# Optimization experiments

Measured on AMD Instinct MI355X. Metric: run time of the kernel, lower is better.

The kernel has to match this reference:

```python
import jax, jax.numpy as jnp
import numpy as np

B, S, D, H, V, C = 64, 512, 512, 512, 32000, 1000
FF = 1024

def setup_inputs() -> dict:
    key = jax.random.key(0)
    ks = jax.random.split(key, 12)
    s = 0.02
    return {
        "tokens": jax.random.randint(ks[0], (B, S), 0, V),
        "emb": jax.random.normal(ks[1], (V, D), jnp.float32) * s,
        "Wx": jax.random.normal(ks[2], (D, H), jnp.float32) * s,
        "Wh": jax.random.normal(ks[3], (H, H), jnp.float32) * s,
        "b_rnn": jnp.zeros((H,), jnp.float32),
        "W1": jax.random.normal(ks[4], (H, FF), jnp.float32) * s,
        "b1": jnp.zeros((FF,), jnp.float32),
        "W2": jax.random.normal(ks[5], (FF, FF), jnp.float32) * s,
        "b2": jnp.zeros((FF,), jnp.float32),
        "Wo": jax.random.normal(ks[6], (FF, C), jnp.float32) * s,
        "bo": jnp.zeros((C,), jnp.float32),
    }

def reference(tokens, emb, Wx, Wh, b_rnn, W1, b1, W2, b2, Wo, bo):
    # Embedding with mask_zero=True: token 0 is a masked timestep
    x = emb[tokens]                                   # [B,S,D]
    mask = (tokens != 0)                              # [B,S]
    # Precompute input projection for all timesteps (hoisted out of the scan)
    xproj = jnp.einsum('bsd,dh->bsh', x, Wx) + b_rnn  # [B,S,H]

    def step(h, inp):
        xp, m = inp                                   # [B,H], [B]
        h_new = jax.nn.relu(xp + h @ Wh)
        # Keras masking: masked steps carry previous state forward
        h = jnp.where(m[:, None], h_new, h)
        return h, None

    h0 = jnp.zeros((B, H), xproj.dtype)
    h, _ = jax.lax.scan(step, h0, (xproj.transpose(1, 0, 2), mask.T))

    y = jax.nn.relu(h @ W1 + b1)
    y = jax.nn.relu(y @ W2 + b2)
    return jax.nn.softmax(y @ Wo + bo, axis=-1)       # [B,C]
```

## Files before the change

kernel.cpp:

```cpp
#include <hip/hip_runtime.h>
#include <stdint.h>

typedef _Float16 half2_t __attribute__((ext_vector_type(2)));
typedef short bf16x8 __attribute__((ext_vector_type(8)));
typedef float f32x4 __attribute__((ext_vector_type(4)));
typedef int i32x4 __attribute__((ext_vector_type(4)));
typedef int i32x8 __attribute__((ext_vector_type(8)));
typedef unsigned short u16;
typedef unsigned int u32;
typedef unsigned long long u64;

#define B_ 64
#define S_ 512
#define D_ 512
#define H_ 512
#define FF_ 1024
#define C_ 1000
#define V_ 32000

#define SW4 128.0f
#define SH4 256.0f

__device__ __forceinline__ u16 f2bf(float f){
  u32 u = __builtin_bit_cast(u32, f);
  u = (u + 0x7FFFu + ((u >> 16) & 1u)) >> 16;
  return (u16)u;
}
__device__ __forceinline__ u32 pkbf(float a, float b){
  return (u32)f2bf(a) | ((u32)f2bf(b) << 16);
}
__device__ __forceinline__ u32 packh2(float a, float b){
  u16 lo = __builtin_bit_cast(u16, (_Float16)a);
  u16 hi = __builtin_bit_cast(u16, (_Float16)b);
  return (u32)lo | ((u32)hi << 16);
}
__device__ __forceinline__ float fdot2u(u32 a, u32 b, float c){
  return __builtin_amdgcn_fdot2(__builtin_bit_cast(half2_t, a),
                                __builtin_bit_cast(half2_t, b), c, false);
}
__device__ __forceinline__ float h2f(u16 h){
  return (float)__builtin_bit_cast(_Float16, h);
}
__device__ __forceinline__ float fp4val(u32 c){
  int e = (c >> 1) & 3;
  float m = 1.0f + 0.5f * (float)(c & 1);
  return (e == 0) ? 0.5f * (float)(c & 1) : m * (float)(1 << (e - 1));
}

__global__ void k_prep(const float* __restrict__ Wx, u16* __restrict__ WxT,
                       const float* __restrict__ Wh, uint4* __restrict__ Wf4){
  __shared__ u16 t[64][65];
  int bid = blockIdx.x, tid = threadIdx.x;
  if (bid < 64){
    int bx = bid & 7, by = bid >> 3;
    int c = tid & 63, r0 = (tid >> 6) * 16;
    #pragma unroll
    for (int i = 0; i < 16; i++){
      int k = by * 64 + r0 + i, n = bx * 64 + c;
      t[r0 + i][c] = f2bf(Wx[k * 512 + n]);
    }
    __syncthreads();
    #pragma unroll
    for (int i = 0; i < 16; i++){
      int n = bx * 64 + r0 + i, k = by * 64 + c;
      WxT[n * 512 + k] = t[c][r0 + i];
    }
  } else {
    int g = (bid - 64) * 256 + tid;
    int fidx = g >> 6, l = g & 63;
    int wv = fidx >> 4, ct = (fidx >> 2) & 3, kt = fidx & 3;
    int q = l >> 4, n = wv * 64 + ct * 16 + (l & 15);
    int k0 = kt * 128 + q * 32;
    u32 d[4] = {0u, 0u, 0u, 0u};
    #pragma unroll
    for (int j = 0; j < 32; j++){
      float w = Wh[(size_t)(k0 + j) * 512 + n] * SW4;
      float aw = fabsf(w);
      u32 s = (w < 0.f) ? 8u : 0u;
      u32 c;
      if (aw < 2.f) c = (u32)(int)rintf(aw * 2.f);
      else if (aw < 4.f) c = 4u + (u32)(int)rintf(aw - 2.f);
      else { c = 6u + (u32)(int)rintf((aw - 4.f) * 0.5f); if (c > 7u) c = 7u; }
      d[j >> 3] |= (c | s) << (4 * (j & 7));
    }
    uint4 o; o.x = d[0]; o.y = d[1]; o.z = d[2]; o.w = d[3];
    Wf4[(size_t)fidx * 64 + l] = o;
  }
}

__global__ __launch_bounds__(512) void k_gemm(const float* __restrict__ emb,
                                              const u16* __restrict__ WxT,
                                              const float* __restrict__ bias,
                                              u16* __restrict__ xpV,
                                              const float* __restrict__ W1, u32* __restrict__ W1p,
                                              const float* __restrict__ W2, u32* __restrict__ W2p,
                                              const float* __restrict__ Wo, u32* __restrict__ Wop){
  __shared__ __align__(16) u16 As[64 * 40];
  int bid = blockIdx.x, tid = threadIdx.x;
  if (bid >= 500){
    if (bid < 1012){
      int i = (bid - 500) * 512 + tid;
      int p = i >> 10, n = i & 1023;
      W1p[p * FF_ + n] = packh2(W1[(2 * p) * FF_ + n], W1[(2 * p + 1) * FF_ + n]);
    } else if (bid < 2036){
      int i = (bid - 1012) * 512 + tid;
      int p = i >> 10, n = i & 1023;
      W2p[p * FF_ + n] = packh2(W2[(2 * p) * FF_ + n], W2[(2 * p + 1) * FF_ + n]);
    } else {
      int i = (bid - 2036) * 512 + tid;
      int p = i >> 10, n = i & 1023;
      if (n < C_)
        Wop[p * C_ + n] = packh2(Wo[(2 * p) * C_ + n], Wo[(2 * p + 1) * C_ + n]);
    }
    return;
  }
  int m0 = bid * 64;
  int w = tid >> 6, l = tid & 63, kg = l >> 4, r16 = l & 15;
  const u16* bptr[4];
  #pragma unroll
  for (int ni = 0; ni < 4; ni++)
    bptr[ni] = WxT + (size_t)(w * 64 + ni * 16 + r16) * 512 + kg * 8;
  f32x4 acc[4][4];
  #pragma unroll
  for (int mi = 0; mi < 4; mi++)
    #pragma unroll
    for (int ni = 0; ni < 4; ni++) acc[mi][ni] = (f32x4){0.f, 0.f, 0.f, 0.f};
  int srow = tid >> 3, sk = (tid & 7) * 4;
  const float* ebase = emb + (size_t)(m0 + srow) * 512 + sk;
  float4 f = *(const float4*)ebase;
  for (int kt = 0; kt < 16; kt++){
    u32 lo = pkbf(f.x, f.y), hi = pkbf(f.z, f.w);
    float4 fn;
    if (kt < 15) fn = *(const float4*)(ebase + (kt + 1) * 32);
    __syncthreads();
    uint2 st; st.x = lo; st.y = hi;
    *(uint2*)(As + srow * 40 + sk) = st;
    __syncthreads();
    bf16x8 bfr[4], af[4];
    #pragma unroll
    for (int ni = 0; ni < 4; ni++)
      bfr[ni] = *(const bf16x8*)(bptr[ni] + kt * 32);
    #pragma unroll
    for (int mi = 0; mi < 4; mi++)
      af[mi] = *(const bf16x8*)(As + (mi * 16 + r16) * 40 + kg * 8);
    #pragma unroll
    for (int mi = 0; mi < 4; mi++)
      #pragma unroll
      for (int ni = 0; ni < 4; ni++)
        acc[mi][ni] = __builtin_amdgcn_mfma_f32_16x16x32_bf16(af[mi], bfr[ni], acc[mi][ni], 0, 0, 0);
    f = fn;
  }
  #pragma unroll
  for (int ni = 0; ni < 4; ni++){
    int col = w * 64 + ni * 16 + r16;
    float bb = bias[col];
    #pragma unroll
    for (int mi = 0; mi < 4; mi++){
      int mb = m0 + mi * 16 + kg * 4;
      #pragma unroll
      for (int r = 0; r < 4; r++){
        float v = (acc[mi][ni][r] + bb) * SH4;
        xpV[(size_t)(mb + r) * 512 + col] = __builtin_bit_cast(u16, (_Float16)v);
      }
    }
  }
}

__global__ __launch_bounds__(512, 2) void k_rnn(
    const uint4* __restrict__ Wf4, const u16* __restrict__ xpV,
    const int* __restrict__ tokens, u32* __restrict__ hpack){
  __shared__ __align__(16) unsigned char gA[256];
  __shared__ __align__(16) unsigned char gB[256];
  __shared__ int toks[512];
  int b = blockIdx.x, tid = threadIdx.x;
  int wv = tid >> 6, l = tid & 63, q = l >> 4, n16 = l & 15;
  int col = wv * 64 + q * 16 + n16;

  i32x8 wgt[16];
  #pragma unroll
  for (int ct = 0; ct < 4; ct++)
    #pragma unroll
    for (int kt = 0; kt < 4; kt++){
      int fidx = (wv * 4 + ct) * 4 + kt;
      uint4 wl = Wf4[(size_t)fidx * 64 + l];
      i32x8 w8 = {(int)wl.x, (int)wl.y, (int)wl.z, (int)wl.w, 0, 0, 0, 0};
      wgt[ct * 4 + kt] = w8;
    }

  toks[tid] = tokens[b * 512 + tid];
  if (tid < 64) ((u32*)gA)[tid] = 0;
  __syncthreads();

  const u16* xpc = xpV + col;
  u16 xraw = xpc[(size_t)toks[0] * 512];
  u32 greg = 0;

#define RNN_STEP(T, SRC, DST)                                                 \
  {                                                                           \
    int tn = toks[(T + 1) & 511];                                             \
    u16 xnext = xpc[(size_t)tn * 512];                                        \
    bool wr = toks[T] != 0;                                                   \
    i32x4 av0 = *(const i32x4*)(SRC + 0 * 64 + q * 16);                       \
    i32x4 av1 = *(const i32x4*)(SRC + 1 * 64 + q * 16);                       \
    i32x4 av2 = *(const i32x4*)(SRC + 2 * 64 + q * 16);                       \
    i32x4 av3 = *(const i32x4*)(SRC + 3 * 64 + q * 16);                       \
    i32x8 a80 = {av0[0], av0[1], av0[2], av0[3], 0, 0, 0, 0};                 \
    i32x8 a81 = {av1[0], av1[1], av1[2], av1[3], 0, 0, 0, 0};                 \
    i32x8 a82 = {av2[0], av2[1], av2[2], av2[3], 0, 0, 0, 0};                 \
    i32x8 a83 = {av3[0], av3[1], av3[2], av3[3], 0, 0, 0, 0};                 \
    f32x4 acc0 = {0.f,0.f,0.f,0.f}, acc1 = {0.f,0.f,0.f,0.f};                 \
    f32x4 acc2 = {0.f,0.f,0.f,0.f}, acc3 = {0.f,0.f,0.f,0.f};                 \
    __builtin_amdgcn_s_setprio(1);                                            \
    acc0 = __builtin_amdgcn_mfma_scale_f32_16x16x128_f8f6f4(a80, wgt[0],  acc0, 4, 4, 0, 127, 0, 127); \
    acc1 = __builtin_amdgcn_mfma_scale_f32_16x16x128_f8f6f4(a80, wgt[4],  acc1, 4, 4, 0, 127, 0, 127); \
    acc2 = __builtin_amdgcn_mfma_scale_f32_16x16x128_f8f6f4(a80, wgt[8],  acc2, 4, 4, 0, 127, 0, 127); \
    acc3 = __builtin_amdgcn_mfma_scale_f32_16x16x128_f8f6f4(a80, wgt[12], acc3, 4, 4, 0, 127, 0, 127); \
    acc0 = __builtin_amdgcn_mfma_scale_f32_16x16x128_f8f6f4(a81, wgt[1],  acc0, 4, 4, 0, 127, 0, 127); \
    acc1 = __builtin_amdgcn_mfma_scale_f32_16x16x128_f8f6f4(a81, wgt[5],  acc1, 4, 4, 0, 127, 0, 127); \
    acc2 = __builtin_amdgcn_mfma_scale_f32_16x16x128_f8f6f4(a81, wgt[9],  acc2, 4, 4, 0, 127, 0, 127); \
    acc3 = __builtin_amdgcn_mfma_scale_f32_16x16x128_f8f6f4(a81, wgt[13], acc3, 4, 4, 0, 127, 0, 127); \
    acc0 = __builtin_amdgcn_mfma_scale_f32_16x16x128_f8f6f4(a82, wgt[2],  acc0, 4, 4, 0, 127, 0, 127); \
    acc1 = __builtin_amdgcn_mfma_scale_f32_16x16x128_f8f6f4(a82, wgt[6],  acc1, 4, 4, 0, 127, 0, 127); \
    acc2 = __builtin_amdgcn_mfma_scale_f32_16x16x128_f8f6f4(a82, wgt[10], acc2, 4, 4, 0, 127, 0, 127); \
    acc3 = __builtin_amdgcn_mfma_scale_f32_16x16x128_f8f6f4(a82, wgt[14], acc3, 4, 4, 0, 127, 0, 127); \
    acc0 = __builtin_amdgcn_mfma_scale_f32_16x16x128_f8f6f4(a83, wgt[3],  acc0, 4, 4, 0, 127, 0, 127); \
    acc1 = __builtin_amdgcn_mfma_scale_f32_16x16x128_f8f6f4(a83, wgt[7],  acc1, 4, 4, 0, 127, 0, 127); \
    acc2 = __builtin_amdgcn_mfma_scale_f32_16x16x128_f8f6f4(a83, wgt[11], acc2, 4, 4, 0, 127, 0, 127); \
    acc3 = __builtin_amdgcn_mfma_scale_f32_16x16x128_f8f6f4(a83, wgt[15], acc3, 4, 4, 0, 127, 0, 127); \
    __builtin_amdgcn_s_setprio(0);                                            \
    float av = (q == 0) ? acc0[0] : (q == 1) ? acc1[0] : (q == 2) ? acc2[0] : acc3[0]; \
    float gn = fmaxf(fmaf(av, 1.0f / SW4, h2f(xraw)), 0.f);                   \
    u32 code;                                                                 \
    if (gn < 2.f) code = (u32)(int)rintf(gn * 2.f);                           \
    else if (gn < 4.f) code = 4u + (u32)(int)rintf(gn - 2.f);                 \
    else { u32 c = 6u + (u32)(int)rintf((gn - 4.f) * 0.5f); code = c > 7u ? 7u : c; } \
    u32 pc = (u32)__shfl_xor((int)code, 1);                                   \
    u32 byte = (n16 & 1) ? (pc | (code << 4)) : (code | (pc << 4));           \
    if (wr) greg = byte;                                                      \
    if ((l & 1) == 0) DST[col >> 1] = (unsigned char)greg;                    \
    xraw = xnext;                                                             \
  }

  #pragma unroll 1
  for (int t = 0; t < 512; t += 2){
    RNN_STEP(t, gA, gB);
    __syncthreads();
    RNN_STEP(t + 1, gB, gA);
    __syncthreads();
  }
#undef RNN_STEP

  if (tid < 256){
    u32 byte = gA[tid];
    float f0 = fp4val(byte & 15u) * (1.0f / SH4);
    float f1 = fp4val(byte >> 4) * (1.0f / SH4);
    hpack[b * 256 + tid] = packh2(f0, f1);
  }
}

__global__ __launch_bounds__(256) void k_fc1(const u32* __restrict__ hpack,
    const u32* __restrict__ W1p, const float* __restrict__ b1, u32* __restrict__ y1p){
  __shared__ u32 h0[256], h1[256];
  int nx = blockIdx.x, bp = blockIdx.y, tid = threadIdx.x;
  int ba = bp * 2, bb = ba + 1;
  int n = nx * 256 + tid;
  h0[tid] = hpack[ba * 256 + tid];
  h1[tid] = hpack[bb * 256 + tid];
  __syncthreads();
  float a0 = 0.f, a1 = 0.f;
  #pragma unroll 8
  for (int p = 0; p < 256; p++){
    u32 w = W1p[p * FF_ + n];
    a0 = fdot2u(w, h0[p], a0);
    a1 = fdot2u(w, h1[p], a1);
  }
  float bbv = b1[n];
  float y0 = fmaxf(a0 + bbv, 0.f), y1 = fmaxf(a1 + bbv, 0.f);
  float o0 = __shfl_xor(y0, 1), o1 = __shfl_xor(y1, 1);
  if (!(tid & 1)){
    y1p[ba * 512 + (n >> 1)] = packh2(y0, o0);
    y1p[bb * 512 + (n >> 1)] = packh2(y1, o1);
  }
}

__global__ __launch_bounds__(256) void k_fc2(const u32* __restrict__ y1p,
    const u32* __restrict__ W2p, const float* __restrict__ b2, u32* __restrict__ y2p){
  __shared__ u32 h0[512], h1[512];
  int nx = blockIdx.x, bp = blockIdx.y, tid = threadIdx.x;
  int ba = bp * 2, bb = ba + 1;
  int n = nx * 256 + tid;
  h0[tid] = y1p[ba * 512 + tid];       h1[tid] = y1p[bb * 512 + tid];
  h0[tid + 256] = y1p[ba * 512 + 256 + tid];
  h1[tid + 256] = y1p[bb * 512 + 256 + tid];
  __syncthreads();
  float a0 = 0.f, a1 = 0.f;
  #pragma unroll 8
  for (int p = 0; p < 512; p++){
    u32 w = W2p[p * FF_ + n];
    a0 = fdot2u(w, h0[p], a0);
    a1 = fdot2u(w, h1[p], a1);
  }
  float bbv = b2[n];
  float y0 = fmaxf(a0 + bbv, 0.f), y1 = fmaxf(a1 + bbv, 0.f);
  float o0 = __shfl_xor(y0, 1), o1 = __shfl_xor(y1, 1);
  if (!(tid & 1)){
    y2p[ba * 512 + (n >> 1)] = packh2(y0, o0);
    y2p[bb * 512 + (n >> 1)] = packh2(y1, o1);
  }
}

__global__ __launch_bounds__(256) void k_outz(const u32* __restrict__ y2p,
    const u32* __restrict__ Wop, const float* __restrict__ bo, float* __restrict__ z){
  __shared__ u32 h0[512], h1[512];
  int nx = blockIdx.x, bp = blockIdx.y, tid = threadIdx.x;
  int ba = bp * 2, bb = ba + 1;
  h0[tid] = y2p[ba * 512 + tid];       h1[tid] = y2p[bb * 512 + tid];
  h0[tid + 256] = y2p[ba * 512 + 256 + tid];
  h1[tid + 256] = y2p[bb * 512 + 256 + tid];
  __syncthreads();
  int n = nx * 250 + tid;
  if (tid >= 250) return;
  float a0 = 0.f, a1 = 0.f;
  #pragma unroll 8
  for (int p = 0; p < 512; p++){
    u32 w = Wop[p * C_ + n];
    a0 = fdot2u(w, h0[p], a0);
    a1 = fdot2u(w, h1[p], a1);
  }
  float bbv = bo[n];
  z[ba * C_ + n] = a0 + bbv;
  z[bb * C_ + n] = a1 + bbv;
}

__global__ __launch_bounds__(256) void k_norm(const float* __restrict__ z,
                                              float* __restrict__ out){
  __shared__ float redm[4], reds[4];
  int b = blockIdx.x, tid = threadIdx.x;
  float z0 = z[b * C_ + tid];
  float z1 = z[b * C_ + 256 + tid];
  float z2 = z[b * C_ + 512 + tid];
  bool v3 = (768 + tid) < C_;
  float z3 = v3 ? z[b * C_ + 768 + tid] : -1e30f;
  float mx = fmaxf(fmaxf(z0, z1), fmaxf(z2, z3));
  #pragma unroll
  for (int o = 1; o < 64; o <<= 1) mx = fmaxf(mx, __shfl_xor(mx, o));
  if ((tid & 63) == 0) redm[tid >> 6] = mx;
  __syncthreads();
  mx = fmaxf(fmaxf(redm[0], redm[1]), fmaxf(redm[2], redm[3]));
  float e0 = __expf(z0 - mx), e1 = __expf(z1 - mx), e2 = __expf(z2 - mx);
  float e3 = v3 ? __expf(z3 - mx) : 0.f;
  float s = e0 + e1 + e2 + e3;
  #pragma unroll
  for (int o = 1; o < 64; o <<= 1) s += __shfl_xor(s, o);
  if ((tid & 63) == 0) reds[tid >> 6] = s;
  __syncthreads();
  s = reds[0] + reds[1] + reds[2] + reds[3];
  float inv = 1.0f / s;
  out[b * C_ + tid] = e0 * inv;
  out[b * C_ + 256 + tid] = e1 * inv;
  out[b * C_ + 512 + tid] = e2 * inv;
  if (v3) out[b * C_ + 768 + tid] = e3 * inv;
}

extern "C" void kernel_launch(void* const* d_in, const int* in_sizes, int n_in,
                              void* d_out, int out_size, void* d_ws, size_t ws_size,
                              hipStream_t stream) {
  const int*   tokens = (const int*)d_in[0];
  const float* emb    = (const float*)d_in[1];
  const float* Wx     = (const float*)d_in[2];
  const float* Wh     = (const float*)d_in[3];
  const float* brnn   = (const float*)d_in[4];
  const float* W1     = (const float*)d_in[5];
  const float* b1     = (const float*)d_in[6];
  const float* W2     = (const float*)d_in[7];
  const float* b2     = (const float*)d_in[8];
  const float* Wo     = (const float*)d_in[9];
  const float* bo     = (const float*)d_in[10];
  float* out = (float*)d_out;

  char* ws = (char*)d_ws;
  size_t off = 0;
  auto alloc = [&](size_t bytes) -> void* {
    void* p = ws + off;
    off += (bytes + 255) & ~(size_t)255;
    return p;
  };
  u16* WxT    = (u16*)alloc((size_t)512 * 512 * 2);
  u16* xpV    = (u16*)alloc((size_t)V_ * 512 * 2);
  uint4* Wf4  = (uint4*)alloc((size_t)128 * 64 * 16);
  u32* W1p    = (u32*)alloc((size_t)256 * 1024 * 4);
  u32* W2p    = (u32*)alloc((size_t)512 * 1024 * 4);
  u32* Wop    = (u32*)alloc((size_t)512 * 1000 * 4);
  u32* hpack  = (u32*)alloc((size_t)64 * 256 * 4);
  u32* y1p    = (u32*)alloc((size_t)64 * 512 * 4);
  u32* y2p    = (u32*)alloc((size_t)64 * 512 * 4);
  float* zbuf = (float*)alloc((size_t)64 * 1000 * 4);

  k_prep<<<dim3(96), dim3(256), 0, stream>>>(Wx, WxT, Wh, Wf4);
  k_gemm<<<dim3(3060), dim3(512), 0, stream>>>(emb, WxT, brnn, xpV,
                                               W1, W1p, W2, W2p, Wo, Wop);
  k_rnn<<<dim3(64), dim3(512), 0, stream>>>(Wf4, xpV, tokens, hpack);
  k_fc1<<<dim3(4, 32), dim3(256), 0, stream>>>(hpack, W1p, b1, y1p);
  k_fc2<<<dim3(4, 32), dim3(256), 0, stream>>>(y1p, W2p, b2, y2p);
  k_outz<<<dim3(4, 32), dim3(256), 0, stream>>>(y2p, Wop, bo, zbuf);
  k_norm<<<dim3(64), dim3(256), 0, stream>>>(zbuf, out);
}
```

Before: 377.3 us.

## Fuse FC1, FC2, output and softmax into one kernel with per-pair barriers

Replaces four tail launches (fc1, fc2, outz, norm) with a single 128-block kernel. Each group of 4 blocks sharing a batch pair synchronizes through a global atomic counter barrier between stages. The counters are zeroed in the gemm kernel. This removes three kernel launch gaps at the cost of spin-wait barriers, which depend on all 128 blocks being co-resident.

Result: slower. 421.9 us (+11.8%).

```diff
diff --git a/kernel.cpp b/kernel.cpp
--- a/kernel.cpp
+++ b/kernel.cpp
@@ -94,10 +94,12 @@
                                               u16* __restrict__ xpV,
                                               const float* __restrict__ W1, u32* __restrict__ W1p,
                                               const float* __restrict__ W2, u32* __restrict__ W2p,
-                                              const float* __restrict__ Wo, u32* __restrict__ Wop){
+                                              const float* __restrict__ Wo, u32* __restrict__ Wop,
+                                              u32* __restrict__ sync){
   __shared__ __align__(16) u16 As[64 * 40];
   int bid = blockIdx.x, tid = threadIdx.x;
   if (bid >= 500){
+    if (bid == 500 && tid < 128) sync[tid] = 0;
     if (bid < 1012){
       int i = (bid - 500) * 512 + tid;
       int p = i >> 10, n = i & 1023;
@@ -258,108 +260,125 @@
   }
 }
 
-__global__ __launch_bounds__(256) void k_fc1(const u32* __restrict__ hpack,
-    const u32* __restrict__ W1p, const float* __restrict__ b1, u32* __restrict__ y1p){
-  __shared__ u32 h0[256], h1[256];
-  int nx = blockIdx.x, bp = blockIdx.y, tid = threadIdx.x;
+__device__ __forceinline__ void pairbar(u32* cnt){
+  __threadfence();
+  __syncthreads();
+  if (threadIdx.x == 0){
+    atomicAdd(cnt, 1u);
+    while (__hip_atomic_load(cnt, __ATOMIC_ACQUIRE, __HIP_MEMORY_SCOPE_AGENT) < 4u)
+      __builtin_amdgcn_s_sleep(1);
+  }
+  __syncthreads();
+  __threadfence();
+}
+
+__global__ __launch_bounds__(256) void k_tail2(const u32* __restrict__ hpack,
+    const u32* __restrict__ W1p, const float* __restrict__ b1,
+    const u32* __restrict__ W2p, const float* __restrict__ b2,
+    const u32* __restrict__ Wop, const float* __restrict__ bo,
+    u32* __restrict__ y1p, u32* __restrict__ y2p,
+    float* __restrict__ zbuf, float* __restrict__ out, u32* __restrict__ sync){
+  __shared__ u32 h0[512], h1[512];
+  __shared__ float redm[4], reds[4];
+  int bid = blockIdx.x, tid = threadIdx.x;
+  int nx = bid & 3, bp = bid >> 2;
   int ba = bp * 2, bb = ba + 1;
-  int n = nx * 256 + tid;
-  h0[tid] = hpack[ba * 256 + tid];
-  h1[tid] = hpack[bb * 256 + tid];
+
+  {
+    h0[tid] = hpack[ba * 256 + tid];
+    h1[tid] = hpack[bb * 256 + tid];
+    __syncthreads();
+    int n = nx * 256 + tid;
+    float a0 = 0.f, a1 = 0.f;
+    #pragma unroll 8
+    for (int p = 0; p < 256; p++){
+      u32 w = W1p[p * FF_ + n];
+      a0 = fdot2u(w, h0[p], a0);
+      a1 = fdot2u(w, h1[p], a1);
+    }
+    float bbv = b1[n];
+    float y0 = fmaxf(a0 + bbv, 0.f), y1 = fmaxf(a1 + bbv, 0.f);
+    float o0 = __shfl_xor(y0, 1), o1 = __shfl_xor(y1, 1);
+    if (!(tid & 1)){
+      y1p[ba * 512 + (n >> 1)] = packh2(y0, o0);
+      y1p[bb * 512 + (n >> 1)] = packh2(y1, o1);
+    }
+  }
+  pairbar(sync + bp);
   __syncthreads();
-  float a0 = 0.f, a1 = 0.f;
-  #pragma unroll 8
-  for (int p = 0; p < 256; p++){
-    u32 w = W1p[p * FF_ + n];
-    a0 = fdot2u(w, h0[p], a0);
-    a1 = fdot2u(w, h1[p], a1);
-  }
-  float bbv = b1[n];
-  float y0 = fmaxf(a0 + bbv, 0.f), y1 = fmaxf(a1 + bbv, 0.f);
-  float o0 = __shfl_xor(y0, 1), o1 = __shfl_xor(y1, 1);
-  if (!(tid & 1)){
-    y1p[ba * 512 + (n >> 1)] = packh2(y0, o0);
-    y1p[bb * 512 + (n >> 1)] = packh2(y1, o1);
-  }
-}
-
-__global__ __launch_bounds__(256) void k_fc2(const u32* __restrict__ y1p,
-    const u32* __restrict__ W2p, const float* __restrict__ b2, u32* __restrict__ y2p){
-  __shared__ u32 h0[512], h1[512];
-  int nx = blockIdx.x, bp = blockIdx.y, tid = threadIdx.x;
-  int ba = bp * 2, bb = ba + 1;
-  int n = nx * 256 + tid;
-  h0[tid] = y1p[ba * 512 + tid];       h1[tid] = y1p[bb * 512 + tid];
-  h0[tid + 256] = y1p[ba * 512 + 256 + tid];
-  h1[tid + 256] = y1p[bb * 512 + 256 + tid];
+
+  {
+    h0[tid] = y1p[ba * 512 + tid];       h1[tid] = y1p[bb * 512 + tid];
+    h0[tid + 256] = y1p[ba * 512 + 256 + tid];
+    h1[tid + 256] = y1p[bb * 512 + 256 + tid];
+    __syncthreads();
+    int n = nx * 256 + tid;
+    float a0 = 0.f, a1 = 0.f;
+    #pragma unroll 8
+    for (int p = 0; p < 512; p++){
+      u32 w = W2p[p * FF_ + n];
+      a0 = fdot2u(w, h0[p], a0);
+      a1 = fdot2u(w, h1[p], a1);
+    }
+    float bbv = b2[n];
+    float y0 = fmaxf(a0 + bbv, 0.f), y1 = fmaxf(a1 + bbv, 0.f);
+    float o0 = __shfl_xor(y0, 1), o1 = __shfl_xor(y1, 1);
+    if (!(tid & 1)){
+      y2p[ba * 512 + (n >> 1)] = packh2(y0, o0);
+      y2p[bb * 512 + (n >> 1)] = packh2(y1, o1);
+    }
+  }
+  pairbar(sync + 32 + bp);
   __syncthreads();
-  float a0 = 0.f, a1 = 0.f;
-  #pragma unroll 8
-  for (int p = 0; p < 512; p++){
-    u32 w = W2p[p * FF_ + n];
-    a0 = fdot2u(w, h0[p], a0);
-    a1 = fdot2u(w, h1[p], a1);
-  }
-  float bbv = b2[n];
-  float y0 = fmaxf(a0 + bbv, 0.f), y1 = fmaxf(a1 + bbv, 0.f);
-  float o0 = __shfl_xor(y0, 1), o1 = __shfl_xor(y1, 1);
-  if (!(tid & 1)){
-    y2p[ba * 512 + (n >> 1)] = packh2(y0, o0);
-    y2p[bb * 512 + (n >> 1)] = packh2(y1, o1);
-  }
-}
-
-__global__ __launch_bounds__(256) void k_outz(const u32* __restrict__ y2p,
-    const u32* __restrict__ Wop, const float* __restrict__ bo, float* __restrict__ z){
-  __shared__ u32 h0[512], h1[512];
-  int nx = blockIdx.x, bp = blockIdx.y, tid = threadIdx.x;
-  int ba = bp * 2, bb = ba + 1;
-  h0[tid] = y2p[ba * 512 + tid];       h1[tid] = y2p[bb * 512 + tid];
-  h0[tid + 256] = y2p[ba * 512 + 256 + tid];
-  h1[tid + 256] = y2p[bb * 512 + 256 + tid];
-  __syncthreads();
-  int n = nx * 250 + tid;
-  if (tid >= 250) return;
-  float a0 = 0.f, a1 = 0.f;
-  #pragma unroll 8
-  for (int p = 0; p < 512; p++){
-    u32 w = Wop[p * C_ + n];
-    a0 = fdot2u(w, h0[p], a0);
-    a1 = fdot2u(w, h1[p], a1);
-  }
-  float bbv = bo[n];
-  z[ba * C_ + n] = a0 + bbv;
-  z[bb * C_ + n] = a1 + bbv;
-}
-
-__global__ __launch_bounds__(256) void k_norm(const float* __restrict__ z,
-                                              float* __restrict__ out){
-  __shared__ float redm[4], reds[4];
-  int b = blockIdx.x, tid = threadIdx.x;
-  float z0 = z[b * C_ + tid];
-  float z1 = z[b * C_ + 256 + tid];
-  float z2 = z[b * C_ + 512 + tid];
-  bool v3 = (768 + tid) < C_;
-  float z3 = v3 ? z[b * C_ + 768 + tid] : -1e30f;
-  float mx = fmaxf(fmaxf(z0, z1), fmaxf(z2, z3));
-  #pragma unroll
-  for (int o = 1; o < 64; o <<= 1) mx = fmaxf(mx, __shfl_xor(mx, o));
-  if ((tid & 63) == 0) redm[tid >> 6] = mx;
-  __syncthreads();
-  mx = fmaxf(fmaxf(redm[0], redm[1]), fmaxf(redm[2], redm[3]));
-  float e0 = __expf(z0 - mx), e1 = __expf(z1 - mx), e2 = __expf(z2 - mx);
-  float e3 = v3 ? __expf(z3 - mx) : 0.f;
-  float s = e0 + e1 + e2 + e3;
-  #pragma unroll
-  for (int o = 1; o < 64; o <<= 1) s += __shfl_xor(s, o);
-  if ((tid & 63) == 0) reds[tid >> 6] = s;
-  __syncthreads();
-  s = reds[0] + reds[1] + reds[2] + reds[3];
-  float inv = 1.0f / s;
-  out[b * C_ + tid] = e0 * inv;
-  out[b * C_ + 256 + tid] = e1 * inv;
-  out[b * C_ + 512 + tid] = e2 * inv;
-  if (v3) out[b * C_ + 768 + tid] = e3 * inv;
+
+  {
+    h0[tid] = y2p[ba * 512 + tid];       h1[tid] = y2p[bb * 512 + tid];
+    h0[tid + 256] = y2p[ba * 512 + 256 + tid];
+    h1[tid + 256] = y2p[bb * 512 + 256 + tid];
+    __syncthreads();
+    if (tid < 250){
+      int n = nx * 250 + tid;
+      float a0 = 0.f, a1 = 0.f;
+      #pragma unroll 8
+      for (int p = 0; p < 512; p++){
+        u32 w = Wop[p * C_ + n];
+        a0 = fdot2u(w, h0[p], a0);
+        a1 = fdot2u(w, h1[p], a1);
+      }
+      float bbv = bo[n];
+      zbuf[ba * C_ + n] = a0 + bbv;
+      zbuf[bb * C_ + n] = a1 + bbv;
+    }
+  }
+  pairbar(sync + 64 + bp);
+
+  if (nx < 2){
+    int b = ba + nx;
+    float z0 = zbuf[b * C_ + tid];
+    float z1 = zbuf[b * C_ + 256 + tid];
+    float z2 = zbuf[b * C_ + 512 + tid];
+    bool v3 = (768 + tid) < C_;
+    float z3 = v3 ? zbuf[b * C_ + 768 + tid] : -1e30f;
+    float mx = fmaxf(fmaxf(z0, z1), fmaxf(z2, z3));
+    #pragma unroll
+    for (int o = 1; o < 64; o <<= 1) mx = fmaxf(mx, __shfl_xor(mx, o));
+    if ((tid & 63) == 0) redm[tid >> 6] = mx;
+    __syncthreads();
+    mx = fmaxf(fmaxf(redm[0], redm[1]), fmaxf(redm[2], redm[3]));
+    float e0 = __expf(z0 - mx), e1 = __expf(z1 - mx), e2 = __expf(z2 - mx);
+    float e3 = v3 ? __expf(z3 - mx) : 0.f;
+    float s = e0 + e1 + e2 + e3;
+    #pragma unroll
+    for (int o = 1; o < 64; o <<= 1) s += __shfl_xor(s, o);
+    if ((tid & 63) == 0) reds[tid >> 6] = s;
+    __syncthreads();
+    s = reds[0] + reds[1] + reds[2] + reds[3];
+    float inv = 1.0f / s;
+    out[b * C_ + tid] = e0 * inv;
+    out[b * C_ + 256 + tid] = e1 * inv;
+    out[b * C_ + 512 + tid] = e2 * inv;
+    if (v3) out[b * C_ + 768 + tid] = e3 * inv;
+  }
 }
 
 extern "C" void kernel_launch(void* const* d_in, const int* in_sizes, int n_in,
@@ -395,13 +414,12 @@
   u32* y1p    = (u32*)alloc((size_t)64 * 512 * 4);
   u32* y2p    = (u32*)alloc((size_t)64 * 512 * 4);
   float* zbuf = (float*)alloc((size_t)64 * 1000 * 4);
+  u32* sync   = (u32*)alloc(512);
 
   k_prep<<<dim3(96), dim3(256), 0, stream>>>(Wx, WxT, Wh, Wf4);
   k_gemm<<<dim3(3060), dim3(512), 0, stream>>>(emb, WxT, brnn, xpV,
-                                               W1, W1p, W2, W2p, Wo, Wop);
+                                               W1, W1p, W2, W2p, Wo, Wop, sync);
   k_rnn<<<dim3(64), dim3(512), 0, stream>>>(Wf4, xpV, tokens, hpack);
-  k_fc1<<<dim3(4, 32), dim3(256), 0, stream>>>(hpack, W1p, b1, y1p);
-  k_fc2<<<dim3(4, 32), dim3(256), 0, stream>>>(y1p, W2p, b2, y2p);
-  k_outz<<<dim3(4, 32), dim3(256), 0, stream>>>(y2p, Wop, bo, zbuf);
-  k_norm<<<dim3(64), dim3(256), 0, stream>>>(zbuf, out);
-}
+  k_tail2<<<dim3(128), dim3(256), 0, stream>>>(hpack, W1p, b1, W2p, b2, Wop, bo,
+                                               y1p, y2p, zbuf, out, sync);
+}
```

## Fuse MLP head and softmax into the RNN kernel tail

Applied to the files above, without the earlier changes.

Folds fc1, fc2, the output projection and the softmax into the end of the RNN kernel, so each of the 64 blocks carries its own batch row through the whole head using shared-memory buffers. This drops four kernel launches and the global round-trips of the intermediate activations. In exchange, the head runs on only 64 blocks, each reading the full weight matrices alone rather than sharing them across a batch pair, so weight traffic per block goes up and parallelism goes down.

New measurement: 380.5 us. No clear change (+0.8%).

```diff
diff --git a/kernel.cpp b/kernel.cpp
--- a/kernel.cpp
+++ b/kernel.cpp
@@ -166,12 +166,19 @@
   }
 }
 
-__global__ __launch_bounds__(512, 2) void k_rnn(
+__global__ __launch_bounds__(512, 2) void k_rnnt(
     const uint4* __restrict__ Wf4, const u16* __restrict__ xpV,
-    const int* __restrict__ tokens, u32* __restrict__ hpack){
+    const int* __restrict__ tokens,
+    const u32* __restrict__ W1p, const float* __restrict__ b1,
+    const u32* __restrict__ W2p, const float* __restrict__ b2,
+    const u32* __restrict__ Wop, const float* __restrict__ bo,
+    float* __restrict__ out){
   __shared__ __align__(16) unsigned char gA[256];
   __shared__ __align__(16) unsigned char gB[256];
   __shared__ int toks[512];
+  __shared__ __align__(16) u32 bufA[512];
+  __shared__ __align__(16) u32 bufB[512];
+  __shared__ float redm[8], reds[8];
   int b = blockIdx.x, tid = threadIdx.x;
   int wv = tid >> 6, l = tid & 63, q = l >> 4, n16 = l & 15;
   int col = wv * 64 + q * 16 + n16;
@@ -254,112 +261,81 @@
     u32 byte = gA[tid];
     float f0 = fp4val(byte & 15u) * (1.0f / SH4);
     float f1 = fp4val(byte >> 4) * (1.0f / SH4);
-    hpack[b * 256 + tid] = packh2(f0, f1);
-  }
-}
-
-__global__ __launch_bounds__(256) void k_fc1(const u32* __restrict__ hpack,
-    const u32* __restrict__ W1p, const float* __restrict__ b1, u32* __restrict__ y1p){
-  __shared__ u32 h0[256], h1[256];
-  int nx = blockIdx.x, bp = blockIdx.y, tid = threadIdx.x;
-  int ba = bp * 2, bb = ba + 1;
-  int n = nx * 256 + tid;
-  h0[tid] = hpack[ba * 256 + tid];
-  h1[tid] = hpack[bb * 256 + tid];
+    bufB[tid] = packh2(f0, f1);
+  }
   __syncthreads();
-  float a0 = 0.f, a1 = 0.f;
-  #pragma unroll 8
-  for (int p = 0; p < 256; p++){
-    u32 w = W1p[p * FF_ + n];
-    a0 = fdot2u(w, h0[p], a0);
-    a1 = fdot2u(w, h1[p], a1);
-  }
-  float bbv = b1[n];
-  float y0 = fmaxf(a0 + bbv, 0.f), y1 = fmaxf(a1 + bbv, 0.f);
-  float o0 = __shfl_xor(y0, 1), o1 = __shfl_xor(y1, 1);
-  if (!(tid & 1)){
-    y1p[ba * 512 + (n >> 1)] = packh2(y0, o0);
-    y1p[bb * 512 + (n >> 1)] = packh2(y1, o1);
-  }
-}
-
-__global__ __launch_bounds__(256) void k_fc2(const u32* __restrict__ y1p,
-    const u32* __restrict__ W2p, const float* __restrict__ b2, u32* __restrict__ y2p){
-  __shared__ u32 h0[512], h1[512];
-  int nx = blockIdx.x, bp = blockIdx.y, tid = threadIdx.x;
-  int ba = bp * 2, bb = ba + 1;
-  int n = nx * 256 + tid;
-  h0[tid] = y1p[ba * 512 + tid];       h1[tid] = y1p[bb * 512 + tid];
-  h0[tid + 256] = y1p[ba * 512 + 256 + tid];
-  h1[tid + 256] = y1p[bb * 512 + 256 + tid];
+
+  {
+    float a0 = 0.f, a1 = 0.f;
+    #pragma unroll 8
+    for (int p = 0; p < 256; p++){
+      u32 h = bufB[p];
+      a0 = fdot2u(W1p[p * FF_ + tid], h, a0);
+      a1 = fdot2u(W1p[p * FF_ + tid + 512], h, a1);
+    }
+    float y0 = fmaxf(a0 + b1[tid], 0.f);
+    float y1 = fmaxf(a1 + b1[tid + 512], 0.f);
+    float o0 = __shfl_xor(y0, 1), o1 = __shfl_xor(y1, 1);
+    if (!(tid & 1)){
+      bufA[tid >> 1] = packh2(y0, o0);
+      bufA[256 + (tid >> 1)] = packh2(y1, o1);
+    }
+  }
   __syncthreads();
-  float a0 = 0.f, a1 = 0.f;
-  #pragma unroll 8
-  for (int p = 0; p < 512; p++){
-    u32 w = W2p[p * FF_ + n];
-    a0 = fdot2u(w, h0[p], a0);
-    a1 = fdot2u(w, h1[p], a1);
-  }
-  float bbv = b2[n];
-  float y0 = fmaxf(a0 + bbv, 0.f), y1 = fmaxf(a1 + bbv, 0.f);
-  float o0 = __shfl_xor(y0, 1), o1 = __shfl_xor(y1, 1);
-  if (!(tid & 1)){
-    y2p[ba * 512 + (n >> 1)] = packh2(y0, o0);
-    y2p[bb * 512 + (n >> 1)] = packh2(y1, o1);
-  }
-}
-
-__global__ __launch_bounds__(256) void k_outz(const u32* __restrict__ y2p,
-    const u32* __restrict__ Wop, const float* __restrict__ bo, float* __restrict__ z){
-  __shared__ u32 h0[512], h1[512];
-  int nx = blockIdx.x, bp = blockIdx.y, tid = threadIdx.x;
-  int ba = bp * 2, bb = ba + 1;
-  h0[tid] = y2p[ba * 512 + tid];       h1[tid] = y2p[bb * 512 + tid];
-  h0[tid + 256] = y2p[ba * 512 + 256 + tid];
-  h1[tid + 256] = y2p[bb * 512 + 256 + tid];
+
+  {
+    float a0 = 0.f, a1 = 0.f;
+    #pragma unroll 8
+    for (int p = 0; p < 512; p++){
+      u32 h = bufA[p];
+      a0 = fdot2u(W2p[p * FF_ + tid], h, a0);
+      a1 = fdot2u(W2p[p * FF_ + tid + 512], h, a1);
+    }
+    float y0 = fmaxf(a0 + b2[tid], 0.f);
+    float y1 = fmaxf(a1 + b2[tid + 512], 0.f);
+    float o0 = __shfl_xor(y0, 1), o1 = __shfl_xor(y1, 1);
+    if (!(tid & 1)){
+      bufB[tid >> 1] = packh2(y0, o0);
+      bufB[256 + (tid >> 1)] = packh2(y1, o1);
+    }
+  }
   __syncthreads();
-  int n = nx * 250 + tid;
-  if (tid >= 250) return;
-  float a0 = 0.f, a1 = 0.f;
-  #pragma unroll 8
-  for (int p = 0; p < 512; p++){
-    u32 w = Wop[p * C_ + n];
-    a0 = fdot2u(w, h0[p], a0);
-    a1 = fdot2u(w, h1[p], a1);
-  }
-  float bbv = bo[n];
-  z[ba * C_ + n] = a0 + bbv;
-  z[bb * C_ + n] = a1 + bbv;
-}
-
-__global__ __launch_bounds__(256) void k_norm(const float* __restrict__ z,
-                                              float* __restrict__ out){
-  __shared__ float redm[4], reds[4];
-  int b = blockIdx.x, tid = threadIdx.x;
-  float z0 = z[b * C_ + tid];
-  float z1 = z[b * C_ + 256 + tid];
-  float z2 = z[b * C_ + 512 + tid];
-  bool v3 = (768 + tid) < C_;
-  float z3 = v3 ? z[b * C_ + 768 + tid] : -1e30f;
-  float mx = fmaxf(fmaxf(z0, z1), fmaxf(z2, z3));
-  #pragma unroll
-  for (int o = 1; o < 64; o <<= 1) mx = fmaxf(mx, __shfl_xor(mx, o));
-  if ((tid & 63) == 0) redm[tid >> 6] = mx;
-  __syncthreads();
-  mx = fmaxf(fmaxf(redm[0], redm[1]), fmaxf(redm[2], redm[3]));
-  float e0 = __expf(z0 - mx), e1 = __expf(z1 - mx), e2 = __expf(z2 - mx);
-  float e3 = v3 ? __expf(z3 - mx) : 0.f;
-  float s = e0 + e1 + e2 + e3;
-  #pragma unroll
-  for (int o = 1; o < 64; o <<= 1) s += __shfl_xor(s, o);
-  if ((tid & 63) == 0) reds[tid >> 6] = s;
-  __syncthreads();
-  s = reds[0] + reds[1] + reds[2] + reds[3];
-  float inv = 1.0f / s;
-  out[b * C_ + tid] = e0 * inv;
-  out[b * C_ + 256 + tid] = e1 * inv;
-  out[b * C_ + 512 + tid] = e2 * inv;
-  if (v3) out[b * C_ + 768 + tid] = e3 * inv;
+
+  {
+    int n0 = tid, n1 = tid + 512;
+    bool v1 = n1 < C_;
+    int n1c = v1 ? n1 : 0;
+    float z0 = 0.f, z1 = 0.f;
+    #pragma unroll 8
+    for (int p = 0; p < 512; p++){
+      u32 y = bufB[p];
+      z0 = fdot2u(Wop[p * C_ + n0], y, z0);
+      z1 = fdot2u(Wop[p * C_ + n1c], y, z1);
+    }
+    z0 += bo[n0];
+    z1 += bo[n1c];
+    float mx = fmaxf(z0, v1 ? z1 : -1e30f);
+    #pragma unroll
+    for (int o = 1; o < 64; o <<= 1) mx = fmaxf(mx, __shfl_xor(mx, o));
+    if ((tid & 63) == 0) redm[wv] = mx;
+    __syncthreads();
+    mx = redm[0];
+    #pragma unroll
+    for (int i = 1; i < 8; i++) mx = fmaxf(mx, redm[i]);
+    float e0 = __expf(z0 - mx);
+    float e1 = v1 ? __expf(z1 - mx) : 0.f;
+    float s = e0 + e1;
+    #pragma unroll
+    for (int o = 1; o < 64; o <<= 1) s += __shfl_xor(s, o);
+    if ((tid & 63) == 0) reds[wv] = s;
+    __syncthreads();
+    s = 0.f;
+    #pragma unroll
+    for (int i = 0; i < 8; i++) s += reds[i];
+    float inv = 1.0f / s;
+    out[(size_t)b * C_ + n0] = e0 * inv;
+    if (v1) out[(size_t)b * C_ + n1] = e1 * inv;
+  }
 }
 
 extern "C" void kernel_launch(void* const* d_in, const int* in_sizes, int n_in,
@@ -391,17 +367,10 @@
   u32* W1p    = (u32*)alloc((size_t)256 * 1024 * 4);
   u32* W2p    = (u32*)alloc((size_t)512 * 1024 * 4);
   u32* Wop    = (u32*)alloc((size_t)512 * 1000 * 4);
-  u32* hpack  = (u32*)alloc((size_t)64 * 256 * 4);
-  u32* y1p    = (u32*)alloc((size_t)64 * 512 * 4);
-  u32* y2p    = (u32*)alloc((size_t)64 * 512 * 4);
-  float* zbuf = (float*)alloc((size_t)64 * 1000 * 4);
 
   k_prep<<<dim3(96), dim3(256), 0, stream>>>(Wx, WxT, Wh, Wf4);
   k_gemm<<<dim3(3060), dim3(512), 0, stream>>>(emb, WxT, brnn, xpV,
                                                W1, W1p, W2, W2p, Wo, Wop);
-  k_rnn<<<dim3(64), dim3(512), 0, stream>>>(Wf4, xpV, tokens, hpack);
-  k_fc1<<<dim3(4, 32), dim3(256), 0, stream>>>(hpack, W1p, b1, y1p);
-  k_fc2<<<dim3(4, 32), dim3(256), 0, stream>>>(y1p, W2p, b2, y2p);
-  k_outz<<<dim3(4, 32), dim3(256), 0, stream>>>(y2p, Wop, bo, zbuf);
-  k_norm<<<dim3(64), dim3(256), 0, stream>>>(zbuf, out);
-}
+  k_rnnt<<<dim3(64), dim3(512), 0, stream>>>(Wf4, xpV, tokens,
+                                             W1p, b1, W2p, b2, Wop, bo, out);
+}
```
